# Optimization experiments

Measured on AMD Instinct MI355X. Metric: run time of the kernel, lower is better.

The kernel has to match this reference:

```python
import jax, jax.numpy as jnp
import numpy as np

N, EM, EW, L, S = 20000, 100000, 25000, 128, 6


def _mlp(x, W1, b1, W2, b2, g, beta):
    # Linear -> ReLU -> Linear -> LayerNorm
    h = jax.nn.relu(x @ W1 + b1) @ W2 + b2
    mu = jnp.mean(h, axis=-1, keepdims=True)
    var = jnp.mean((h - mu) ** 2, axis=-1, keepdims=True)
    return g * (h - mu) * jax.lax.rsqrt(var + 1e-5) + beta


def _scatter_mean(attr, recv, n):
    s = jax.ops.segment_sum(attr, recv, num_segments=n)
    c = jax.ops.segment_sum(jnp.ones((attr.shape[0], 1), attr.dtype), recv, num_segments=n)
    return s / jnp.maximum(c, 1.0)


def setup_inputs() -> dict:
    key = jax.random.key(0)
    ks = jax.random.split(key, 16)

    def w(k, shape, fan_in):
        return (jax.random.normal(k, shape, jnp.float32) / np.sqrt(fan_in).astype(np.float32))

    inp = {
        'x': jax.random.normal(ks[0], (N, L), jnp.float32),
        'mesh_edge_attr': jax.random.normal(ks[1], (EM, L), jnp.float32),
        'world_edge_attr': jax.random.normal(ks[2], (EW, L), jnp.float32),
        'mesh_edge_index': jax.random.randint(ks[3], (2, EM), 0, N),
        'world_edge_index': jax.random.randint(ks[4], (2, EW), 0, N),
    }
    i = 5
    for pre in ('me', 'we', 'nd'):
        inp[pre + '_W1'] = w(ks[i], (S, 3 * L, L), 3 * L); i += 1
        inp[pre + '_b1'] = jnp.zeros((S, L), jnp.float32)
        inp[pre + '_W2'] = w(ks[i], (S, L, L), L); i += 1
        inp[pre + '_b2'] = jnp.zeros((S, L), jnp.float32)
        inp[pre + '_g'] = jnp.ones((S, L), jnp.float32)
        inp[pre + '_beta'] = jnp.zeros((S, L), jnp.float32)
    return inp


def reference(x, mesh_edge_attr, world_edge_attr, mesh_edge_index, world_edge_index,
              me_W1, me_b1, me_W2, me_b2, me_g, me_beta,
              we_W1, we_b1, we_W2, we_b2, we_g, we_beta,
              nd_W1, nd_b1, nd_W2, nd_b2, nd_g, nd_beta):
    ms, mr = mesh_edge_index[0], mesh_edge_index[1]
    ws, wr = world_edge_index[0], world_edge_index[1]
    n = x.shape[0]

    def step(carry, p):
        x, mea, wea = carry
        (mW1, mb1, mW2, mb2, mg, mbe,
         wW1, wb1, wW2, wb2, wg, wbe,
         nW1, nb1, nW2, nb2, ng, nbe) = p
        # EdgeModel: gather + concat + MLP, residual into edge attrs
        mea = mea + _mlp(jnp.concatenate([x[ms], x[mr], mea], axis=-1), mW1, mb1, mW2, mb2, mg, mbe)
        wea = wea + _mlp(jnp.concatenate([x[ws], x[wr], wea], axis=-1), wW1, wb1, wW2, wb2, wg, wbe)
        # NodeModel: scatter-mean over both edge sets + concat + MLP, residual
        agg = jnp.concatenate([x, _scatter_mean(mea, mr, n), _scatter_mean(wea, wr, n)], axis=-1)
        x = x + _mlp(agg, nW1, nb1, nW2, nb2, ng, nbe)
        return (x, mea, wea), None

    params = (me_W1, me_b1, me_W2, me_b2, me_g, me_beta,
              we_W1, we_b1, we_W2, we_b2, we_g, we_beta,
              nd_W1, nd_b1, nd_W2, nd_b2, nd_g, nd_beta)
    (x, mea, wea), _ = jax.lax.scan(step, (x, mesh_edge_attr, world_edge_attr), params)
    return x, mea, wea
```

## Files before the change

### kernel.cpp

```cpp
#include <hip/hip_runtime.h>

constexpr int LDIM  = 128;
constexpr int NNODE = 20000;
constexpr int EM_N  = 100000;
constexpr int EW_N  = 25000;
constexpr int NSTEP = 6;

typedef short bf16x8 __attribute__((ext_vector_type(8)));
typedef short bf16x4 __attribute__((ext_vector_type(4)));
typedef float f32x4  __attribute__((ext_vector_type(4)));

struct MlpParams {
  const short* xb;
  const float* attrIn;
  float*       attrOut;
  short*       xbOut;
  const int*   src;
  const int*   dst;
  const int*   oidx;
  float*       origOut;
  const float* gsrc1;
  const float* gsrc2;
  const int*   off1;
  const int*   csr1;
  const int*   off2;
  const int*   csr2;
  const short* W1H;
  const short* W2H;
  const short* W2L;
  const float* b1;
  const float* b2;
  const float* gam;
  const float* bet;
  int nRows;
};

__device__ __forceinline__ short f2b(float f) {
  unsigned int u = __float_as_uint(f);
  u = (u + 0x7fffu + ((u >> 16) & 1u)) >> 16;
  return (short)u;
}
__device__ __forceinline__ float b2f(short s) {
  return __uint_as_float(((unsigned int)(unsigned short)s) << 16);
}
__device__ __forceinline__ bf16x4 cvt4(float4 a, float sc) {
  bf16x4 o;
  o[0] = f2b(a.x * sc); o[1] = f2b(a.y * sc);
  o[2] = f2b(a.z * sc); o[3] = f2b(a.w * sc);
  return o;
}
__device__ __forceinline__ bf16x4 cvt4v(f32x4 a, float sc) {
  bf16x4 o;
  o[0] = f2b(a[0] * sc); o[1] = f2b(a[1] * sc);
  o[2] = f2b(a[2] * sc); o[3] = f2b(a[3] * sc);
  return o;
}

__launch_bounds__(256, 2)
__global__ void edge_kernel(MlpParams pmA, MlpParams pmB, int blocksA) {
  const bool isA = (int)blockIdx.x < blocksA;
  const MlpParams P = isA ? pmA : pmB;
  const int bid  = isA ? (int)blockIdx.x : (int)blockIdx.x - blocksA;
  const int row0 = bid * 128;

  __shared__ __align__(16) short Abuf[128][40];
  __shared__ __align__(16) short Bhi[128][40];
  __shared__ __align__(16) short Blo[128][40];
  __shared__ __align__(16) short Hbuf[128][136];
  __shared__ float b1s[128], b2s[128], gs[128], bes[128];
  __shared__ int   idxa[128], idxb[128];
  __shared__ float sumL[2][128], sqL[2][128];
  __shared__ float muL[128], rsL[128];

  const int t = threadIdx.x;

  if (t < 128) {
    b1s[t] = P.b1[t];
    gs[t]  = P.gam[t];
    int r = row0 + t;
    idxa[t] = (r < P.nRows) ? P.src[r] : 0;
  } else {
    int t2 = t - 128;
    b2s[t2] = P.b2[t2];
    bes[t2] = P.bet[t2];
    int r = row0 + t2;
    idxb[t2] = (r < P.nRows) ? P.dst[r] : 0;
  }
  __syncthreads();

  const int l   = t & 63;
  const int wid = t >> 6;
  const int wr  = wid >> 1, wcc = wid & 1;
  const int lr  = l & 15,  lg  = l >> 4;

  const int  srow  = t >> 1, sh = t & 1;
  const int  sgRow = row0 + srow;
  const bool sval  = sgRow < P.nRows;
  const int  sgC   = sval ? sgRow : 0;
  const float vmask = sval ? 1.f : 0.f;

  const short* bx0   = P.xb + (size_t)idxa[srow] * LDIM + sh * 16;
  const short* bx1   = P.xb + (size_t)idxb[srow] * LDIM + sh * 16;
  const float* base2 = P.attrIn + (size_t)sgC * LDIM + sh * 16;

  const int wrow = t >> 1, wsh = t & 1;
  const short* w1base = P.W1H + (size_t)wrow * 384 + wsh * 16;

  f32x4 acc[4][4];
#pragma unroll
  for (int i = 0; i < 4; ++i)
#pragma unroll
    for (int j = 0; j < 4; ++j) acc[i][j] = f32x4{0.f, 0.f, 0.f, 0.f};

  const bf16x8 z8 = {0, 0, 0, 0, 0, 0, 0, 0};
  bf16x8 pB0, pB1;
  float4 pA0, pA1, pA2, pA3;
  bf16x8 pW0, pW1;
  {
    pB0 = *(const bf16x8*)bx0;
    pB1 = *(const bf16x8*)(bx0 + 8);
    pW0 = *(const bf16x8*)w1base;
    pW1 = *(const bf16x8*)(w1base + 8);
  }

#pragma unroll
  for (int kc = 0; kc < 12; ++kc) {
    const int seg = kc >> 2;
    if (kc > 0) __syncthreads();
    {
      if (seg < 2) {
        *(bf16x8*)&Abuf[srow][sh * 16]     = sval ? pB0 : z8;
        *(bf16x8*)&Abuf[srow][sh * 16 + 8] = sval ? pB1 : z8;
      } else {
        *(bf16x4*)&Abuf[srow][sh * 16 + 0]  = cvt4(pA0, vmask);
        *(bf16x4*)&Abuf[srow][sh * 16 + 4]  = cvt4(pA1, vmask);
        *(bf16x4*)&Abuf[srow][sh * 16 + 8]  = cvt4(pA2, vmask);
        *(bf16x4*)&Abuf[srow][sh * 16 + 12] = cvt4(pA3, vmask);
      }
      *(bf16x8*)&Bhi[wrow][wsh * 16]     = pW0;
      *(bf16x8*)&Bhi[wrow][wsh * 16 + 8] = pW1;
    }
    __syncthreads();
    if (kc < 11) {
      const int kn = kc + 1, segn = kn >> 2, partn = kn & 3;
      if (segn == 0) {
        pB0 = *(const bf16x8*)(bx0 + partn * 32);
        pB1 = *(const bf16x8*)(bx0 + partn * 32 + 8);
      } else if (segn == 1) {
        pB0 = *(const bf16x8*)(bx1 + partn * 32);
        pB1 = *(const bf16x8*)(bx1 + partn * 32 + 8);
      } else {
        const float4* bp = (const float4*)(base2 + partn * 32);
        pA0 = bp[0]; pA1 = bp[1]; pA2 = bp[2]; pA3 = bp[3];
      }
      pW0 = *(const bf16x8*)(w1base + kn * 32);
      pW1 = *(const bf16x8*)(w1base + kn * 32 + 8);
    }
    bf16x8 av[4], bh[4];
#pragma unroll
    for (int mi = 0; mi < 4; ++mi)
      av[mi] = *(const bf16x8*)&Abuf[wr * 64 + mi * 16 + lr][lg * 8];
#pragma unroll
    for (int ni = 0; ni < 4; ++ni)
      bh[ni] = *(const bf16x8*)&Bhi[wcc * 64 + ni * 16 + lr][lg * 8];
#pragma unroll
    for (int mi = 0; mi < 4; ++mi)
#pragma unroll
      for (int ni = 0; ni < 4; ++ni)
        acc[mi][ni] = __builtin_amdgcn_mfma_f32_16x16x32_bf16(av[mi], bh[ni], acc[mi][ni], 0, 0, 0);
  }

#pragma unroll
  for (int rt = 0; rt < 4; ++rt)
#pragma unroll
    for (int ct = 0; ct < 4; ++ct) {
      const int cc = wcc * 64 + ct * 16 + lr;
      const float bb = b1s[cc];
#pragma unroll
      for (int q = 0; q < 4; ++q) {
        const int rr = wr * 64 + rt * 16 + lg * 4 + q;
        Hbuf[rr][cc] = f2b(fmaxf(acc[rt][ct][q] + bb, 0.f));
      }
    }

  f32x4 acc2[4][4];
#pragma unroll
  for (int i = 0; i < 4; ++i)
#pragma unroll
    for (int j = 0; j < 4; ++j) acc2[i][j] = f32x4{0.f, 0.f, 0.f, 0.f};

  const short* w2hbase = P.W2H + (size_t)wrow * 128 + wsh * 16;
  const short* w2lbase = P.W2L + (size_t)wrow * 128 + wsh * 16;

  bf16x8 qh0 = *(const bf16x8*)w2hbase;
  bf16x8 qh1 = *(const bf16x8*)(w2hbase + 8);
  bf16x8 ql0 = *(const bf16x8*)w2lbase;
  bf16x8 ql1 = *(const bf16x8*)(w2lbase + 8);

#pragma unroll
  for (int kc = 0; kc < 4; ++kc) {
    __syncthreads();
    {
      *(bf16x8*)&Bhi[wrow][wsh * 16]     = qh0;
      *(bf16x8*)&Bhi[wrow][wsh * 16 + 8] = qh1;
      *(bf16x8*)&Blo[wrow][wsh * 16]     = ql0;
      *(bf16x8*)&Blo[wrow][wsh * 16 + 8] = ql1;
    }
    __syncthreads();
    if (kc < 3) {
      qh0 = *(const bf16x8*)(w2hbase + (kc + 1) * 32);
      qh1 = *(const bf16x8*)(w2hbase + (kc + 1) * 32 + 8);
      ql0 = *(const bf16x8*)(w2lbase + (kc + 1) * 32);
      ql1 = *(const bf16x8*)(w2lbase + (kc + 1) * 32 + 8);
    }
    bf16x8 av2[4], bh2[4], bl2[4];
#pragma unroll
    for (int rt = 0; rt < 4; ++rt)
      av2[rt] = *(const bf16x8*)&Hbuf[wr * 64 + rt * 16 + lr][kc * 32 + lg * 8];
#pragma unroll
    for (int ct = 0; ct < 4; ++ct) {
      bh2[ct] = *(const bf16x8*)&Bhi[wcc * 64 + ct * 16 + lr][lg * 8];
      bl2[ct] = *(const bf16x8*)&Blo[wcc * 64 + ct * 16 + lr][lg * 8];
    }
#pragma unroll
    for (int rt = 0; rt < 4; ++rt)
#pragma unroll
      for (int ct = 0; ct < 4; ++ct) {
        acc2[rt][ct] = __builtin_amdgcn_mfma_f32_16x16x32_bf16(av2[rt], bl2[ct], acc2[rt][ct], 0, 0, 0);
        acc2[rt][ct] = __builtin_amdgcn_mfma_f32_16x16x32_bf16(av2[rt], bh2[ct], acc2[rt][ct], 0, 0, 0);
      }
  }

  float s1[4][4], s2[4][4];
#pragma unroll
  for (int rt = 0; rt < 4; ++rt)
#pragma unroll
    for (int q = 0; q < 4; ++q) { s1[rt][q] = 0.f; s2[rt][q] = 0.f; }
#pragma unroll
  for (int rt = 0; rt < 4; ++rt)
#pragma unroll
    for (int ct = 0; ct < 4; ++ct) {
      const float bb = b2s[wcc * 64 + ct * 16 + lr];
#pragma unroll
      for (int q = 0; q < 4; ++q) {
        float v = acc2[rt][ct][q] + bb;
        acc2[rt][ct][q] = v;
        s1[rt][q] += v;
        s2[rt][q] += v * v;
      }
    }
#pragma unroll
  for (int m = 1; m < 16; m <<= 1) {
#pragma unroll
    for (int rt = 0; rt < 4; ++rt)
#pragma unroll
      for (int q = 0; q < 4; ++q) {
        s1[rt][q] += __shfl_xor(s1[rt][q], m);
        s2[rt][q] += __shfl_xor(s2[rt][q], m);
      }
  }
  __syncthreads();
  {
    const int rt = lr >> 2, q = lr & 3;
    const int rr = wr * 64 + rt * 16 + lg * 4 + q;
    sumL[wcc][rr] = s1[rt][q];
    sqL[wcc][rr]  = s2[rt][q];
  }
  __syncthreads();
  if (t < 128) {
    const float tot = sumL[0][t] + sumL[1][t];
    const float tsq = sqL[0][t] + sqL[1][t];
    const float mu  = tot * (1.0f / 128.0f);
    const float var = tsq * (1.0f / 128.0f) - mu * mu;
    muL[t] = mu;
    rsL[t] = rsqrtf(var + 1e-5f);
  }
  __syncthreads();

#pragma unroll
  for (int rt = 0; rt < 4; ++rt) {
#pragma unroll
    for (int q = 0; q < 4; ++q) {
      const int rr = wr * 64 + rt * 16 + lg * 4 + q;
      const int grow = row0 + rr;
      if (grow < P.nRows) {
        const float mu = muL[rr], rs = rsL[rr];
        const float* rin = P.attrIn + (size_t)grow * LDIM;
        float* rout = P.attrOut + (size_t)grow * LDIM;
        float* rout2 = nullptr;
        if (P.origOut) rout2 = P.origOut + (size_t)P.oidx[grow] * LDIM;
#pragma unroll
        for (int ct = 0; ct < 4; ++ct) {
          const int cc = wcc * 64 + ct * 16 + lr;
          const float o = gs[cc] * (acc2[rt][ct][q] - mu) * rs + bes[cc] + rin[cc];
          rout[cc] = o;
          if (rout2) rout2[cc] = o;
        }
      }
    }
  }
}

template<bool CONTIG>
__launch_bounds__(256, 2)
__global__ void node_kernel(MlpParams P) {
  const int bid  = (int)blockIdx.x;
  const int row0 = bid * 128;

  __shared__ __align__(16) short Abuf[128][40];
  __shared__ __align__(16) short Bhi[128][40];
  __shared__ __align__(16) short Blo[128][40];
  __shared__ __align__(16) short Hbuf[128][136];
  __shared__ float b1s[128], b2s[128], gs[128], bes[128];
  __shared__ float sumL[2][128], sqL[2][128];
  __shared__ float muL[128], rsL[128];

  const int t = threadIdx.x;
  if (t < 128) { b1s[t] = P.b1[t]; gs[t] = P.gam[t]; }
  else         { b2s[t - 128] = P.b2[t - 128]; bes[t - 128] = P.bet[t - 128]; }

  const int l   = t & 63;
  const int wid = t >> 6;
  const int wr  = wid >> 1, wcc = wid & 1;
  const int lr  = l & 15,  lg  = l >> 4;

  const int  srow  = t >> 1, sh = t & 1;
  const int  sgRow = row0 + srow;
  const bool sval  = sgRow < P.nRows;
  const int  sgC   = sval ? sgRow : 0;

  const int wrow = t >> 1, wsh = t & 1;
  const short* w1base = P.W1H + (size_t)wrow * 384 + wsh * 16;
  const short* xrow   = P.xb + (size_t)sgC * LDIM + sh * 16;
  const bf16x8 z8 = {0, 0, 0, 0, 0, 0, 0, 0};

  f32x4 acc[4][4];
#pragma unroll
  for (int i = 0; i < 4; ++i)
#pragma unroll
    for (int j = 0; j < 4; ++j) acc[i][j] = f32x4{0.f, 0.f, 0.f, 0.f};

  f32x4 g[16];
#pragma unroll
  for (int j = 0; j < 16; ++j) g[j] = f32x4{0.f, 0.f, 0.f, 0.f};
  float scm = 1.f;
  {
    int beg = 0, end = 0;
    if (sval) { beg = P.off1[sgRow]; end = P.off1[sgRow + 1]; }
    for (int i = beg; i < end; ++i) {
      const size_t r = CONTIG ? (size_t)i : (size_t)P.csr1[i];
      const float* er = P.gsrc1 + r * LDIM + sh * 16;
#pragma unroll
      for (int part = 0; part < 4; ++part) {
        const f32x4* p = (const f32x4*)(er + part * 32);
#pragma unroll
        for (int j = 0; j < 4; ++j) g[part * 4 + j] += p[j];
      }
    }
    scm = 1.0f / (float)max(end - beg, 1);
  }

  __syncthreads();

  float scw = 1.f;
#pragma unroll
  for (int kc = 0; kc < 12; ++kc) {
    const int seg = kc >> 2, part = kc & 3;
    if (kc > 0) __syncthreads();
    {
      if (seg == 0) {
        const bf16x8* xp = (const bf16x8*)(xrow + part * 32);
        *(bf16x8*)&Abuf[srow][sh * 16]     = sval ? xp[0] : z8;
        *(bf16x8*)&Abuf[srow][sh * 16 + 8] = sval ? xp[1] : z8;
      } else {
        const float sc = (seg == 1) ? scm : scw;
        *(bf16x4*)&Abuf[srow][sh * 16 + 0]  = cvt4v(g[part * 4 + 0], sc);
        *(bf16x4*)&Abuf[srow][sh * 16 + 4]  = cvt4v(g[part * 4 + 1], sc);
        *(bf16x4*)&Abuf[srow][sh * 16 + 8]  = cvt4v(g[part * 4 + 2], sc);
        *(bf16x4*)&Abuf[srow][sh * 16 + 12] = cvt4v(g[part * 4 + 3], sc);
      }
      const short* wsrc = w1base + kc * 32;
      *(bf16x8*)&Bhi[wrow][wsh * 16]     = *(const bf16x8*)wsrc;
      *(bf16x8*)&Bhi[wrow][wsh * 16 + 8] = *(const bf16x8*)(wsrc + 8);
      if (kc == 7) {
#pragma unroll
        for (int j = 0; j < 16; ++j) g[j] = f32x4{0.f, 0.f, 0.f, 0.f};
        int beg = 0, end = 0;
        if (sval) { beg = P.off2[sgRow]; end = P.off2[sgRow + 1]; }
        for (int i = beg; i < end; ++i) {
          const size_t r = CONTIG ? (size_t)i : (size_t)P.csr2[i];
          const float* er = P.gsrc2 + r * LDIM + sh * 16;
#pragma unroll
          for (int pp = 0; pp < 4; ++pp) {
            const f32x4* p = (const f32x4*)(er + pp * 32);
#pragma unroll
            for (int j = 0; j < 4; ++j) g[pp * 4 + j] += p[j];
          }
        }
        scw = 1.0f / (float)max(end - beg, 1);
      }
    }
    __syncthreads();
    bf16x8 av[4], bh[4];
#pragma unroll
    for (int mi = 0; mi < 4; ++mi)
      av[mi] = *(const bf16x8*)&Abuf[wr * 64 + mi * 16 + lr][lg * 8];
#pragma unroll
    for (int ni = 0; ni < 4; ++ni)
      bh[ni] = *(const bf16x8*)&Bhi[wcc * 64 + ni * 16 + lr][lg * 8];
#pragma unroll
    for (int mi = 0; mi < 4; ++mi)
#pragma unroll
      for (int ni = 0; ni < 4; ++ni)
        acc[mi][ni] = __builtin_amdgcn_mfma_f32_16x16x32_bf16(av[mi], bh[ni], acc[mi][ni], 0, 0, 0);
  }

#pragma unroll
  for (int rt = 0; rt < 4; ++rt)
#pragma unroll
    for (int ct = 0; ct < 4; ++ct) {
      const int cc = wcc * 64 + ct * 16 + lr;
      const float bb = b1s[cc];
#pragma unroll
      for (int q = 0; q < 4; ++q) {
        const int rr = wr * 64 + rt * 16 + lg * 4 + q;
        Hbuf[rr][cc] = f2b(fmaxf(acc[rt][ct][q] + bb, 0.f));
      }
    }

  f32x4 acc2[4][4];
#pragma unroll
  for (int i = 0; i < 4; ++i)
#pragma unroll
    for (int j = 0; j < 4; ++j) acc2[i][j] = f32x4{0.f, 0.f, 0.f, 0.f};

  const short* w2hbase = P.W2H + (size_t)wrow * 128 + wsh * 16;
  const short* w2lbase = P.W2L + (size_t)wrow * 128 + wsh * 16;
  bf16x8 qh0 = *(const bf16x8*)w2hbase;
  bf16x8 qh1 = *(const bf16x8*)(w2hbase + 8);
  bf16x8 ql0 = *(const bf16x8*)w2lbase;
  bf16x8 ql1 = *(const bf16x8*)(w2lbase + 8);

#pragma unroll
  for (int kc = 0; kc < 4; ++kc) {
    __syncthreads();
    {
      *(bf16x8*)&Bhi[wrow][wsh * 16]     = qh0;
      *(bf16x8*)&Bhi[wrow][wsh * 16 + 8] = qh1;
      *(bf16x8*)&Blo[wrow][wsh * 16]     = ql0;
      *(bf16x8*)&Blo[wrow][wsh * 16 + 8] = ql1;
    }
    __syncthreads();
    if (kc < 3) {
      qh0 = *(const bf16x8*)(w2hbase + (kc + 1) * 32);
      qh1 = *(const bf16x8*)(w2hbase + (kc + 1) * 32 + 8);
      ql0 = *(const bf16x8*)(w2lbase + (kc + 1) * 32);
      ql1 = *(const bf16x8*)(w2lbase + (kc + 1) * 32 + 8);
    }
    bf16x8 av2[4], bh2[4], bl2[4];
#pragma unroll
    for (int rt = 0; rt < 4; ++rt)
      av2[rt] = *(const bf16x8*)&Hbuf[wr * 64 + rt * 16 + lr][kc * 32 + lg * 8];
#pragma unroll
    for (int ct = 0; ct < 4; ++ct) {
      bh2[ct] = *(const bf16x8*)&Bhi[wcc * 64 + ct * 16 + lr][lg * 8];
      bl2[ct] = *(const bf16x8*)&Blo[wcc * 64 + ct * 16 + lr][lg * 8];
    }
#pragma unroll
    for (int rt = 0; rt < 4; ++rt)
#pragma unroll
      for (int ct = 0; ct < 4; ++ct) {
        acc2[rt][ct] = __builtin_amdgcn_mfma_f32_16x16x32_bf16(av2[rt], bl2[ct], acc2[rt][ct], 0, 0, 0);
        acc2[rt][ct] = __builtin_amdgcn_mfma_f32_16x16x32_bf16(av2[rt], bh2[ct], acc2[rt][ct], 0, 0, 0);
      }
  }

  float s1[4][4], s2[4][4];
#pragma unroll
  for (int rt = 0; rt < 4; ++rt)
#pragma unroll
    for (int q = 0; q < 4; ++q) { s1[rt][q] = 0.f; s2[rt][q] = 0.f; }
#pragma unroll
  for (int rt = 0; rt < 4; ++rt)
#pragma unroll
    for (int ct = 0; ct < 4; ++ct) {
      const float bb = b2s[wcc * 64 + ct * 16 + lr];
#pragma unroll
      for (int q = 0; q < 4; ++q) {
        float v = acc2[rt][ct][q] + bb;
        acc2[rt][ct][q] = v;
        s1[rt][q] += v;
        s2[rt][q] += v * v;
      }
    }
#pragma unroll
  for (int m = 1; m < 16; m <<= 1) {
#pragma unroll
    for (int rt = 0; rt < 4; ++rt)
#pragma unroll
      for (int q = 0; q < 4; ++q) {
        s1[rt][q] += __shfl_xor(s1[rt][q], m);
        s2[rt][q] += __shfl_xor(s2[rt][q], m);
      }
  }
  __syncthreads();
  {
    const int rt = lr >> 2, q = lr & 3;
    const int rr = wr * 64 + rt * 16 + lg * 4 + q;
    sumL[wcc][rr] = s1[rt][q];
    sqL[wcc][rr]  = s2[rt][q];
  }
  __syncthreads();
  if (t < 128) {
    const float tot = sumL[0][t] + sumL[1][t];
    const float tsq = sqL[0][t] + sqL[1][t];
    const float mu  = tot * (1.0f / 128.0f);
    const float var = tsq * (1.0f / 128.0f) - mu * mu;
    muL[t] = mu;
    rsL[t] = rsqrtf(var + 1e-5f);
  }
  __syncthreads();

#pragma unroll
  for (int rt = 0; rt < 4; ++rt) {
#pragma unroll
    for (int q = 0; q < 4; ++q) {
      const int rr = wr * 64 + rt * 16 + lg * 4 + q;
      const int grow = row0 + rr;
      if (grow < P.nRows) {
        const float mu = muL[rr], rs = rsL[rr];
        const float* rin = P.attrIn + (size_t)grow * LDIM;
        float* rout = P.attrOut + (size_t)grow * LDIM;
        short* xbo  = P.xbOut + (size_t)grow * LDIM;
#pragma unroll
        for (int ct = 0; ct < 4; ++ct) {
          const int cc = wcc * 64 + ct * 16 + lr;
          const float o = gs[cc] * (acc2[rt][ct][q] - mu) * rs + bes[cc] + rin[cc];
          rout[cc] = o;
          xbo[cc] = f2b(o);
        }
      }
    }
  }
}

__global__ void prep_weights(const float* w1a, const float* w1b, const float* w1c,
                             const float* w2a, const float* w2b, const float* w2c,
                             short* w1h, short* w2h, short* w2l) {
  int i = blockIdx.x * 256 + threadIdx.x;
  constexpr int N1 = 18 * 128 * 384;
  constexpr int N2 = 18 * 128 * 128;
  if (i < N1) {
    int g = i / (128 * 384);
    int rem = i - g * (128 * 384);
    int n = rem / 384, k = rem - n * 384;
    int m = g / 6, s = g - m * 6;
    const float* src = (m == 0) ? w1a : (m == 1) ? w1b : w1c;
    w1h[i] = f2b(src[(size_t)s * (384 * 128) + (size_t)k * 128 + n]);
  } else if (i < N1 + N2) {
    int j = i - N1;
    int g = j / (128 * 128);
    int rem = j - g * (128 * 128);
    int n = rem / 128, k = rem - n * 128;
    int m = g / 6, s = g - m * 6;
    const float* src = (m == 0) ? w2a : (m == 1) ? w2b : w2c;
    float f = src[(size_t)s * (128 * 128) + (size_t)k * 128 + n];
    short hi = f2b(f);
    w2h[j] = hi;
    w2l[j] = f2b(f - b2f(hi));
  }
}

__global__ void prep_xb(const float* x, short* xb) {
  int i = blockIdx.x * 256 + threadIdx.x;
  if (i < NNODE * LDIM) xb[i] = f2b(x[i]);
}

__global__ void prep_deg(const int* mr, const int* wrcv, int* degm, int* degw) {
  int i = blockIdx.x * 256 + threadIdx.x;
  if (i < EM_N) atomicAdd(&degm[mr[i]], 1);
  else if (i < EM_N + EW_N) atomicAdd(&degw[wrcv[i - EM_N]], 1);
}

__global__ void prep_scan(const int* degm, const int* degw, int* moff, int* woff) {
  __shared__ int part[256];
  const int t = threadIdx.x;
  constexpr int NPT = (NNODE + 255) / 256;
#pragma unroll 1
  for (int pass = 0; pass < 2; ++pass) {
    const int* deg = pass == 0 ? degm : degw;
    int* off = pass == 0 ? moff : woff;
    int s = 0;
    for (int i = 0; i < NPT; ++i) {
      int n = t * NPT + i;
      if (n < NNODE) s += deg[n];
    }
    part[t] = s;
    __syncthreads();
    for (int d = 1; d < 256; d <<= 1) {
      int v = (t >= d) ? part[t - d] : 0;
      __syncthreads();
      part[t] += v;
      __syncthreads();
    }
    int base = (t == 0) ? 0 : part[t - 1];
    for (int i = 0; i < NPT; ++i) {
      int n = t * NPT + i;
      if (n < NNODE) { off[n] = base; base += deg[n]; }
    }
    if (t == 255) off[NNODE] = base;
    __syncthreads();
  }
}

__global__ void prep_fill(const int* ms, const int* mr, const int* wsnd, const int* wrcv,
                          const int* moff, const int* woff,
                          int* mcur, int* wcur, int* mcsr, int* wcsr,
                          int* psm, int* pdm, int* psw, int* pdw) {
  int i = blockIdx.x * 256 + threadIdx.x;
  if (i < EM_N) {
    int d = mr[i];
    int pos = moff[d] + atomicAdd(&mcur[d], 1);
    mcsr[pos] = i;
    psm[pos] = ms[i];
    pdm[pos] = d;
  } else if (i < EM_N + EW_N) {
    int j = i - EM_N;
    int d = wrcv[j];
    int pos = woff[d] + atomicAdd(&wcur[d], 1);
    wcsr[pos] = j;
    psw[pos] = wsnd[j];
    pdw[pos] = d;
  }
}

__global__ void prep_permute(const float* src_m, const float* src_w,
                             const int* mcsr, const int* wcsr,
                             float* dst_m, float* dst_w) {
  long i = (long)blockIdx.x * 256 + threadIdx.x;
  const long NM4 = (long)EM_N * 32, NW4 = (long)EW_N * 32;
  if (i < NM4) {
    long pos = i >> 5, c = i & 31;
    ((float4*)dst_m)[pos * 32 + c] = ((const float4*)src_m)[(size_t)mcsr[pos] * 32 + c];
  } else if (i < NM4 + NW4) {
    long j = i - NM4;
    long pos = j >> 5, c = j & 31;
    ((float4*)dst_w)[pos * 32 + c] = ((const float4*)src_w)[(size_t)wcsr[pos] * 32 + c];
  }
}

extern "C" void kernel_launch(void* const* d_in, const int* in_sizes, int n_in,
                              void* d_out, int out_size, void* d_ws, size_t ws_size,
                              hipStream_t stream) {
  (void)in_sizes; (void)n_in; (void)out_size;
  const float* x_in   = (const float*)d_in[0];
  const float* mea_in = (const float*)d_in[1];
  const float* wea_in = (const float*)d_in[2];
  const int*   mei    = (const int*)d_in[3];
  const int*   wei    = (const int*)d_in[4];
  const float* W1s[3] = { (const float*)d_in[5],  (const float*)d_in[11], (const float*)d_in[17] };
  const float* B1s[3] = { (const float*)d_in[6],  (const float*)d_in[12], (const float*)d_in[18] };
  const float* W2s[3] = { (const float*)d_in[7],  (const float*)d_in[13], (const float*)d_in[19] };
  const float* B2s[3] = { (const float*)d_in[8],  (const float*)d_in[14], (const float*)d_in[20] };
  const float* Gs[3]  = { (const float*)d_in[9],  (const float*)d_in[15], (const float*)d_in[21] };
  const float* Be[3]  = { (const float*)d_in[10], (const float*)d_in[16], (const float*)d_in[22] };

  float* xo  = (float*)d_out;
  float* meo = xo  + (size_t)NNODE * LDIM;
  float* weo = meo + (size_t)EM_N * LDIM;

  const size_t SORT_BYTES = ((size_t)EM_N + EW_N) * LDIM * 4;
  const size_t SMALL_BYTES = (size_t)20 * 1024 * 1024;
  const bool SORTED = ws_size >= SORT_BYTES + SMALL_BYTES;

  float* msort = (float*)d_ws;
  float* wsort = msort + (size_t)EM_N * LDIM;
  short* w1h = SORTED ? (short*)(wsort + (size_t)EW_N * LDIM) : (short*)d_ws;
  short* w2h = w1h + (size_t)18 * 128 * 384;
  short* w2l = w2h + (size_t)18 * 128 * 128;
  short* xb  = w2l + (size_t)18 * 128 * 128;
  int* degm = (int*)(xb + (size_t)NNODE * LDIM);
  int* degw = degm + NNODE;
  int* mcur = degw + NNODE;
  int* wcur = mcur + NNODE;
  int* moff = wcur + NNODE;
  int* woff = moff + (NNODE + 1);
  int* mcsr = woff + (NNODE + 1);
  int* wcsr = mcsr + EM_N;
  int* psm  = wcsr + EW_N;
  int* pdm  = psm + EM_N;
  int* psw  = pdm + EM_N;
  int* pdw  = psw + EW_N;

  hipMemsetAsync(degm, 0, (size_t)4 * NNODE * 4, stream);

  {
    int tot = 18 * 128 * 384 + 18 * 128 * 128;
    prep_weights<<<dim3((tot + 255) / 256), 256, 0, stream>>>(
        W1s[0], W1s[1], W1s[2], W2s[0], W2s[1], W2s[2], w1h, w2h, w2l);
  }
  prep_xb<<<dim3((NNODE * LDIM + 255) / 256), 256, 0, stream>>>(x_in, xb);
  prep_deg<<<dim3((EM_N + EW_N + 255) / 256), 256, 0, stream>>>(mei + EM_N, wei + EW_N, degm, degw);
  prep_scan<<<dim3(1), 256, 0, stream>>>(degm, degw, moff, woff);
  prep_fill<<<dim3((EM_N + EW_N + 255) / 256), 256, 0, stream>>>(
      mei, mei + EM_N, wei, wei + EW_N, moff, woff, mcur, wcur, mcsr, wcsr,
      psm, pdm, psw, pdw);
  if (SORTED) {
    long tot4 = ((long)EM_N + EW_N) * 32;
    prep_permute<<<dim3((unsigned)((tot4 + 255) / 256)), 256, 0, stream>>>(
        mea_in, wea_in, mcsr, wcsr, msort, wsort);
  }

  const int MB = (EM_N + 127) / 128;
  const int WB = (EW_N + 127) / 128;
  const int NB = (NNODE + 127) / 128;

  const float* mc = mea_in;
  const float* wc = wea_in;
  const float* xc = x_in;

  for (int s = 0; s < NSTEP; ++s) {
    MlpParams pm{}, pw{}, pn{};
    const bool last = (s == NSTEP - 1);

    pm.xb = xb;
    pm.W1H = w1h + (size_t)(0 * 6 + s) * 128 * 384;
    pm.W2H = w2h + (size_t)(0 * 6 + s) * 128 * 128;
    pm.W2L = w2l + (size_t)(0 * 6 + s) * 128 * 128;
    pm.b1 = B1s[0] + s * LDIM; pm.b2 = B2s[0] + s * LDIM;
    pm.gam = Gs[0] + s * LDIM; pm.bet = Be[0] + s * LDIM;
    pm.nRows = EM_N;

    pw.xb = xb;
    pw.W1H = w1h + (size_t)(1 * 6 + s) * 128 * 384;
    pw.W2H = w2h + (size_t)(1 * 6 + s) * 128 * 128;
    pw.W2L = w2l + (size_t)(1 * 6 + s) * 128 * 128;
    pw.b1 = B1s[1] + s * LDIM; pw.b2 = B2s[1] + s * LDIM;
    pw.gam = Gs[1] + s * LDIM; pw.bet = Be[1] + s * LDIM;
    pw.nRows = EW_N;

    if (SORTED) {
      pm.attrIn = msort; pm.attrOut = msort;
      pm.src = psm; pm.dst = pdm;
      pm.oidx = mcsr; pm.origOut = last ? meo : nullptr;
      pw.attrIn = wsort; pw.attrOut = wsort;
      pw.src = psw; pw.dst = pdw;
      pw.oidx = wcsr; pw.origOut = last ? weo : nullptr;
    } else {
      pm.attrIn = mc; pm.attrOut = meo;
      pm.src = mei; pm.dst = mei + EM_N;
      pw.attrIn = wc; pw.attrOut = weo;
      pw.src = wei; pw.dst = wei + EW_N;
    }

    edge_kernel<<<dim3(MB + WB), 256, 0, stream>>>(pm, pw, MB);

    pn.xb = xb; pn.attrIn = xc; pn.attrOut = xo; pn.xbOut = xb;
    pn.off1 = moff; pn.off2 = woff;
    pn.W1H = w1h + (size_t)(2 * 6 + s) * 128 * 384;
    pn.W2H = w2h + (size_t)(2 * 6 + s) * 128 * 128;
    pn.W2L = w2l + (size_t)(2 * 6 + s) * 128 * 128;
    pn.b1 = B1s[2] + s * LDIM; pn.b2 = B2s[2] + s * LDIM;
    pn.gam = Gs[2] + s * LDIM; pn.bet = Be[2] + s * LDIM;
    pn.nRows = NNODE;

    if (SORTED) {
      pn.gsrc1 = msort; pn.gsrc2 = wsort;
      node_kernel<true><<<dim3(NB), 256, 0, stream>>>(pn);
    } else {
      pn.gsrc1 = meo; pn.gsrc2 = weo;
      pn.csr1 = mcsr; pn.csr2 = wcsr;
      node_kernel<false><<<dim3(NB), 256, 0, stream>>>(pn);
    }

    mc = meo; wc = weo; xc = xo;
  }
}
```

Before: 852.5 us.

## Shrink node kernel row tile to 32 and split aggregation across 8 threads per row

The node MLP kernel now processes 32 rows per block instead of 128, so the grid grows from 157 to 625 blocks. Each row's scatter-mean gather is now split across 8 threads, each reading one 16-float slice, instead of 2 threads each reading four 32-float parts. Each wave computes all 32 rows times a 32-column slice, and occupancy is raised to 3 blocks per CU. The aim is to spread the latency-bound CSR gathers over more threads and blocks to fill the GPU better. The cost is that every block reloads the full W1/W2 weights for only 32 rows, and there are fewer MFMAs per LDS load.

```diff
diff --git a/kernel.cpp b/kernel.cpp
--- a/kernel.cpp
+++ b/kernel.cpp
@@ -302,60 +302,55 @@
 }
 
 template<bool CONTIG>
-__launch_bounds__(256, 2)
+__launch_bounds__(256, 3)
 __global__ void node_kernel(MlpParams P) {
-  const int bid  = (int)blockIdx.x;
-  const int row0 = bid * 128;
-
-  __shared__ __align__(16) short Abuf[128][40];
+  constexpr int BR = 32;
+  const int row0 = (int)blockIdx.x * BR;
+
+  __shared__ __align__(16) short Abuf[BR][40];
   __shared__ __align__(16) short Bhi[128][40];
   __shared__ __align__(16) short Blo[128][40];
-  __shared__ __align__(16) short Hbuf[128][136];
+  __shared__ __align__(16) short Hbuf[BR][136];
   __shared__ float b1s[128], b2s[128], gs[128], bes[128];
-  __shared__ float sumL[2][128], sqL[2][128];
-  __shared__ float muL[128], rsL[128];
+  __shared__ float sumL[4][BR], sqL[4][BR], muL[BR], rsL[BR];
 
   const int t = threadIdx.x;
   if (t < 128) { b1s[t] = P.b1[t]; gs[t] = P.gam[t]; }
   else         { b2s[t - 128] = P.b2[t - 128]; bes[t - 128] = P.bet[t - 128]; }
 
-  const int l   = t & 63;
-  const int wid = t >> 6;
-  const int wr  = wid >> 1, wcc = wid & 1;
-  const int lr  = l & 15,  lg  = l >> 4;
-
-  const int  srow  = t >> 1, sh = t & 1;
+  const int l  = t & 63;
+  const int w  = t >> 6;
+  const int lr = l & 15, lg = l >> 4;
+
+  const int  srow  = t >> 3, sh = t & 7;
   const int  sgRow = row0 + srow;
   const bool sval  = sgRow < P.nRows;
   const int  sgC   = sval ? sgRow : 0;
+  const int  myPart = sh >> 1, myHalf = sh & 1;
 
   const int wrow = t >> 1, wsh = t & 1;
   const short* w1base = P.W1H + (size_t)wrow * 384 + wsh * 16;
   const short* xrow   = P.xb + (size_t)sgC * LDIM + sh * 16;
   const bf16x8 z8 = {0, 0, 0, 0, 0, 0, 0, 0};
 
-  f32x4 acc[4][4];
-#pragma unroll
-  for (int i = 0; i < 4; ++i)
-#pragma unroll
-    for (int j = 0; j < 4; ++j) acc[i][j] = f32x4{0.f, 0.f, 0.f, 0.f};
-
-  f32x4 g[16];
-#pragma unroll
-  for (int j = 0; j < 16; ++j) g[j] = f32x4{0.f, 0.f, 0.f, 0.f};
+  f32x4 acc[2][2];
+#pragma unroll
+  for (int i = 0; i < 2; ++i)
+#pragma unroll
+    for (int j = 0; j < 2; ++j) acc[i][j] = f32x4{0.f, 0.f, 0.f, 0.f};
+
+  f32x4 g[4];
+#pragma unroll
+  for (int j = 0; j < 4; ++j) g[j] = f32x4{0.f, 0.f, 0.f, 0.f};
   float scm = 1.f;
   {
     int beg = 0, end = 0;
     if (sval) { beg = P.off1[sgRow]; end = P.off1[sgRow + 1]; }
     for (int i = beg; i < end; ++i) {
       const size_t r = CONTIG ? (size_t)i : (size_t)P.csr1[i];
-      const float* er = P.gsrc1 + r * LDIM + sh * 16;
-#pragma unroll
-      for (int part = 0; part < 4; ++part) {
-        const f32x4* p = (const f32x4*)(er + part * 32);
-#pragma unroll
-        for (int j = 0; j < 4; ++j) g[part * 4 + j] += p[j];
-      }
+      const f32x4* p = (const f32x4*)(P.gsrc1 + r * LDIM + sh * 16);
+#pragma unroll
+      for (int j = 0; j < 4; ++j) g[j] += p[j];
     }
     scm = 1.0f / (float)max(end - beg, 1);
   }
@@ -368,71 +363,69 @@
     const int seg = kc >> 2, part = kc & 3;
     if (kc > 0) __syncthreads();
     {
-      if (seg == 0) {
-        const bf16x8* xp = (const bf16x8*)(xrow + part * 32);
-        *(bf16x8*)&Abuf[srow][sh * 16]     = sval ? xp[0] : z8;
-        *(bf16x8*)&Abuf[srow][sh * 16 + 8] = sval ? xp[1] : z8;
-      } else {
-        const float sc = (seg == 1) ? scm : scw;
-        *(bf16x4*)&Abuf[srow][sh * 16 + 0]  = cvt4v(g[part * 4 + 0], sc);
-        *(bf16x4*)&Abuf[srow][sh * 16 + 4]  = cvt4v(g[part * 4 + 1], sc);
-        *(bf16x4*)&Abuf[srow][sh * 16 + 8]  = cvt4v(g[part * 4 + 2], sc);
-        *(bf16x4*)&Abuf[srow][sh * 16 + 12] = cvt4v(g[part * 4 + 3], sc);
+      if (myPart == part) {
+        if (seg == 0) {
+          const bf16x8* xp = (const bf16x8*)xrow;
+          *(bf16x8*)&Abuf[srow][myHalf * 16]     = sval ? xp[0] : z8;
+          *(bf16x8*)&Abuf[srow][myHalf * 16 + 8] = sval ? xp[1] : z8;
+        } else {
+          const float sc = (seg == 1) ? scm : scw;
+          *(bf16x4*)&Abuf[srow][myHalf * 16 + 0]  = cvt4v(g[0], sc);
+          *(bf16x4*)&Abuf[srow][myHalf * 16 + 4]  = cvt4v(g[1], sc);
+          *(bf16x4*)&Abuf[srow][myHalf * 16 + 8]  = cvt4v(g[2], sc);
+          *(bf16x4*)&Abuf[srow][myHalf * 16 + 12] = cvt4v(g[3], sc);
+        }
       }
       const short* wsrc = w1base + kc * 32;
       *(bf16x8*)&Bhi[wrow][wsh * 16]     = *(const bf16x8*)wsrc;
       *(bf16x8*)&Bhi[wrow][wsh * 16 + 8] = *(const bf16x8*)(wsrc + 8);
       if (kc == 7) {
 #pragma unroll
-        for (int j = 0; j < 16; ++j) g[j] = f32x4{0.f, 0.f, 0.f, 0.f};
+        for (int j = 0; j < 4; ++j) g[j] = f32x4{0.f, 0.f, 0.f, 0.f};
         int beg = 0, end = 0;
         if (sval) { beg = P.off2[sgRow]; end = P.off2[sgRow + 1]; }
         for (int i = beg; i < end; ++i) {
           const size_t r = CONTIG ? (size_t)i : (size_t)P.csr2[i];
-          const float* er = P.gsrc2 + r * LDIM + sh * 16;
-#pragma unroll
-          for (int pp = 0; pp < 4; ++pp) {
-            const f32x4* p = (const f32x4*)(er + pp * 32);
-#pragma unroll
-            for (int j = 0; j < 4; ++j) g[pp * 4 + j] += p[j];
-          }
+          const f32x4* p = (const f32x4*)(P.gsrc2 + r * LDIM + sh * 16);
+#pragma unroll
+          for (int j = 0; j < 4; ++j) g[j] += p[j];
         }
         scw = 1.0f / (float)max(end - beg, 1);
       }
     }
     __syncthreads();
-    bf16x8 av[4], bh[4];
-#pragma unroll
-    for (int mi = 0; mi < 4; ++mi)
-      av[mi] = *(const bf16x8*)&Abuf[wr * 64 + mi * 16 + lr][lg * 8];
-#pragma unroll
-    for (int ni = 0; ni < 4; ++ni)
-      bh[ni] = *(const bf16x8*)&Bhi[wcc * 64 + ni * 16 + lr][lg * 8];
-#pragma unroll
-    for (int mi = 0; mi < 4; ++mi)
-#pragma unroll
-      for (int ni = 0; ni < 4; ++ni)
+    bf16x8 av[2], bh[2];
+#pragma unroll
+    for (int mi = 0; mi < 2; ++mi)
+      av[mi] = *(const bf16x8*)&Abuf[mi * 16 + lr][lg * 8];
+#pragma unroll
+    for (int ni = 0; ni < 2; ++ni)
+      bh[ni] = *(const bf16x8*)&Bhi[w * 32 + ni * 16 + lr][lg * 8];
+#pragma unroll
+    for (int mi = 0; mi < 2; ++mi)
+#pragma unroll
+      for (int ni = 0; ni < 2; ++ni)
         acc[mi][ni] = __builtin_amdgcn_mfma_f32_16x16x32_bf16(av[mi], bh[ni], acc[mi][ni], 0, 0, 0);
   }
 
 #pragma unroll
-  for (int rt = 0; rt < 4; ++rt)
-#pragma unroll
-    for (int ct = 0; ct < 4; ++ct) {
-      const int cc = wcc * 64 + ct * 16 + lr;
+  for (int mi = 0; mi < 2; ++mi)
+#pragma unroll
+    for (int ni = 0; ni < 2; ++ni) {
+      const int cc = w * 32 + ni * 16 + lr;
       const float bb = b1s[cc];
 #pragma unroll
       for (int q = 0; q < 4; ++q) {
-        const int rr = wr * 64 + rt * 16 + lg * 4 + q;
-        Hbuf[rr][cc] = f2b(fmaxf(acc[rt][ct][q] + bb, 0.f));
-      }
-    }
-
-  f32x4 acc2[4][4];
-#pragma unroll
-  for (int i = 0; i < 4; ++i)
-#pragma unroll
-    for (int j = 0; j < 4; ++j) acc2[i][j] = f32x4{0.f, 0.f, 0.f, 0.f};
+        const int rr = mi * 16 + lg * 4 + q;
+        Hbuf[rr][cc] = f2b(fmaxf(acc[mi][ni][q] + bb, 0.f));
+      }
+    }
+
+  f32x4 acc2[2][2];
+#pragma unroll
+  for (int i = 0; i < 2; ++i)
+#pragma unroll
+    for (int j = 0; j < 2; ++j) acc2[i][j] = f32x4{0.f, 0.f, 0.f, 0.f};
 
   const short* w2hbase = P.W2H + (size_t)wrow * 128 + wsh * 16;
   const short* w2lbase = P.W2L + (size_t)wrow * 128 + wsh * 16;
@@ -457,63 +450,64 @@
       ql0 = *(const bf16x8*)(w2lbase + (kc + 1) * 32);
       ql1 = *(const bf16x8*)(w2lbase + (kc + 1) * 32 + 8);
     }
-    bf16x8 av2[4], bh2[4], bl2[4];
-#pragma unroll
-    for (int rt = 0; rt < 4; ++rt)
-      av2[rt] = *(const bf16x8*)&Hbuf[wr * 64 + rt * 16 + lr][kc * 32 + lg * 8];
-#pragma unroll
-    for (int ct = 0; ct < 4; ++ct) {
-      bh2[ct] = *(const bf16x8*)&Bhi[wcc * 64 + ct * 16 + lr][lg * 8];
-      bl2[ct] = *(const bf16x8*)&Blo[wcc * 64 + ct * 16 + lr][lg * 8];
-    }
-#pragma unroll
-    for (int rt = 0; rt < 4; ++rt)
-#pragma unroll
-      for (int ct = 0; ct < 4; ++ct) {
-        acc2[rt][ct] = __builtin_amdgcn_mfma_f32_16x16x32_bf16(av2[rt], bl2[ct], acc2[rt][ct], 0, 0, 0);
-        acc2[rt][ct] = __builtin_amdgcn_mfma_f32_16x16x32_bf16(av2[rt], bh2[ct], acc2[rt][ct], 0, 0, 0);
-      }
-  }
-
-  float s1[4][4], s2[4][4];
-#pragma unroll
-  for (int rt = 0; rt < 4; ++rt)
-#pragma unroll
-    for (int q = 0; q < 4; ++q) { s1[rt][q] = 0.f; s2[rt][q] = 0.f; }
-#pragma unroll
-  for (int rt = 0; rt < 4; ++rt)
-#pragma unroll
-    for (int ct = 0; ct < 4; ++ct) {
-      const float bb = b2s[wcc * 64 + ct * 16 + lr];
+    bf16x8 av2[2], bh2[2], bl2[2];
+#pragma unroll
+    for (int mi = 0; mi < 2; ++mi)
+      av2[mi] = *(const bf16x8*)&Hbuf[mi * 16 + lr][kc * 32 + lg * 8];
+#pragma unroll
+    for (int ni = 0; ni < 2; ++ni) {
+      bh2[ni] = *(const bf16x8*)&Bhi[w * 32 + ni * 16 + lr][lg * 8];
+      bl2[ni] = *(const bf16x8*)&Blo[w * 32 + ni * 16 + lr][lg * 8];
+    }
+#pragma unroll
+    for (int mi = 0; mi < 2; ++mi)
+#pragma unroll
+      for (int ni = 0; ni < 2; ++ni) {
+        acc2[mi][ni] = __builtin_amdgcn_mfma_f32_16x16x32_bf16(av2[mi], bl2[ni], acc2[mi][ni], 0, 0, 0);
+        acc2[mi][ni] = __builtin_amdgcn_mfma_f32_16x16x32_bf16(av2[mi], bh2[ni], acc2[mi][ni], 0, 0, 0);
+      }
+  }
+
+  float s1[2][4], s2[2][4];
+#pragma unroll
+  for (int mi = 0; mi < 2; ++mi)
+#pragma unroll
+    for (int q = 0; q < 4; ++q) { s1[mi][q] = 0.f; s2[mi][q] = 0.f; }
+#pragma unroll
+  for (int mi = 0; mi < 2; ++mi)
+#pragma unroll
+    for (int ni = 0; ni < 2; ++ni) {
+      const float bb = b2s[w * 32 + ni * 16 + lr];
 #pragma unroll
       for (int q = 0; q < 4; ++q) {
-        float v = acc2[rt][ct][q] + bb;
-        acc2[rt][ct][q] = v;
-        s1[rt][q] += v;
-        s2[rt][q] += v * v;
+        float v = acc2[mi][ni][q] + bb;
+        acc2[mi][ni][q] = v;
+        s1[mi][q] += v;
+        s2[mi][q] += v * v;
       }
     }
 #pragma unroll
   for (int m = 1; m < 16; m <<= 1) {
 #pragma unroll
-    for (int rt = 0; rt < 4; ++rt)
+    for (int mi = 0; mi < 2; ++mi)
 #pragma unroll
       for (int q = 0; q < 4; ++q) {
-        s1[rt][q] += __shfl_xor(s1[rt][q], m);
-        s2[rt][q] += __shfl_xor(s2[rt][q], m);
+        s1[mi][q] += __shfl_xor(s1[mi][q], m);
+        s2[mi][q] += __shfl_xor(s2[mi][q], m);
       }
   }
   __syncthreads();
-  {
-    const int rt = lr >> 2, q = lr & 3;
-    const int rr = wr * 64 + rt * 16 + lg * 4 + q;
-    sumL[wcc][rr] = s1[rt][q];
-    sqL[wcc][rr]  = s2[rt][q];
+  if (lr < 8) {
+    const int mi = lr >> 2, q = lr & 3;
+    const int rr = mi * 16 + lg * 4 + q;
+    sumL[w][rr] = s1[mi][q];
+    sqL[w][rr]  = s2[mi][q];
   }
   __syncthreads();
-  if (t < 128) {
-    const float tot = sumL[0][t] + sumL[1][t];
-    const float tsq = sqL[0][t] + sqL[1][t];
+  if (t < BR) {
+    float tot = 0.f, tsq = 0.f;
+#pragma unroll
+    for (int ww = 0; ww < 4; ++ww) { tot += sumL[ww][t]; tsq += sqL[ww][t]; }
     const float mu  = tot * (1.0f / 128.0f);
     const float var = tsq * (1.0f / 128.0f) - mu * mu;
     muL[t] = mu;
@@ -522,10 +516,10 @@
   __syncthreads();
 
 #pragma unroll
-  for (int rt = 0; rt < 4; ++rt) {
+  for (int mi = 0; mi < 2; ++mi) {
 #pragma unroll
     for (int q = 0; q < 4; ++q) {
-      const int rr = wr * 64 + rt * 16 + lg * 4 + q;
+      const int rr = mi * 16 + lg * 4 + q;
       const int grow = row0 + rr;
       if (grow < P.nRows) {
         const float mu = muL[rr], rs = rsL[rr];
@@ -533,9 +527,9 @@
         float* rout = P.attrOut + (size_t)grow * LDIM;
         short* xbo  = P.xbOut + (size_t)grow * LDIM;
 #pragma unroll
-        for (int ct = 0; ct < 4; ++ct) {
-          const int cc = wcc * 64 + ct * 16 + lr;
-          const float o = gs[cc] * (acc2[rt][ct][q] - mu) * rs + bes[cc] + rin[cc];
+        for (int ni = 0; ni < 2; ++ni) {
+          const int cc = w * 32 + ni * 16 + lr;
+          const float o = gs[cc] * (acc2[mi][ni][q] - mu) * rs + bes[cc] + rin[cc];
           rout[cc] = o;
           xbo[cc] = f2b(o);
         }
@@ -713,7 +707,7 @@
 
   const int MB = (EM_N + 127) / 128;
   const int WB = (EW_N + 127) / 128;
-  const int NB = (NNODE + 127) / 128;
+  const int NB = (NNODE + 31) / 32;
 
   const float* mc = mea_in;
   const float* wc = wea_in;
```

Measured after the change: 805.7 us. -5.5%, faster.
